# Kernel optimization log

Measured on AMD Instinct MI355X. Metric: run time of the kernel, lower is better.

Reference implementation:

```python
import jax, jax.numpy as jnp
import numpy as np
import math

B, C, L, K, DIL = 8, 32, 32768, 11, 10
PAD_SAME = math.ceil(DIL * (K - 1) / 2)   # 'same' padding for deformable conv
PAD_OFF = (K - 1) // 2                    # padding for the offset-predicting conv
EPS = 1e-3


def batchnorm(x, gamma, beta, mean, var):
    # eval-mode BN over channel dim of [B, C, L]
    scale = (gamma / jnp.sqrt(var + EPS))[None, :, None]
    return (x - mean[None, :, None]) * scale + beta[None, :, None]


def conv1d(x, w, b, pad):
    # x: [B, Cin, L], w: [Cout, Cin, K]
    y = jax.lax.conv_general_dilated(x, w, (1,), [(pad, pad)],
                                     dimension_numbers=('NCH', 'OIH', 'NCH'))
    return y + b[None, :, None]


def deform_conv1d(x, offset, w, b, dilation, pad):
    # x: [B, C, L]; offset: [B, L, K] (single offset group); w: [Cout, Cin, K]
    Bn, Cn, Ln = x.shape
    Kn = w.shape[-1]
    base = jnp.arange(Ln, dtype=x.dtype)[:, None] + jnp.arange(Kn, dtype=x.dtype)[None, :] * dilation - pad
    pos = base[None, :, :] + offset                       # [B, L, K] fractional sample positions
    lo = jnp.floor(pos)
    frac = pos - lo
    lo_i = lo.astype(jnp.int32)

    def gather(idx):
        valid = ((idx >= 0) & (idx < Ln)).astype(x.dtype)  # zero padding outside
        idxc = jnp.clip(idx, 0, Ln - 1).reshape(Bn, 1, Ln * Kn)
        g = jnp.take_along_axis(x, idxc, axis=2).reshape(Bn, Cn, Ln, Kn)
        return g * valid[:, None, :, :]

    v_lo = gather(lo_i)
    v_hi = gather(lo_i + 1)
    sampled = v_lo * (1.0 - frac)[:, None, :, :] + v_hi * frac[:, None, :, :]  # [B, C, L, K]
    out = jnp.einsum('bclk,ock->bol', sampled, w) + b[None, :, None]
    return out


def setup_inputs() -> dict:
    key = jax.random.key(0)
    ks = jax.random.split(key, 8)
    f32 = jnp.float32
    small = lambda k, shape: jax.random.normal(k, shape, dtype=f32) * 0.05
    return dict(
        x=jax.random.normal(ks[0], (B, C, L), dtype=f32),
        bn1_gamma=jnp.ones((C,), f32), bn1_beta=jnp.zeros((C,), f32),
        bn1_mean=small(ks[1], (C,)),
        bn1_var=jax.random.uniform(ks[2], (C,), dtype=f32, minval=0.5, maxval=1.5),
        bn2_gamma=jnp.ones((C,), f32), bn2_beta=jnp.zeros((C,), f32),
        bn2_mean=small(ks[3], (C,)),
        bn2_var=jax.random.uniform(ks[4], (C,), dtype=f32, minval=0.5, maxval=1.5),
        off1_w=small(ks[5], (K, C, K)), off1_b=jnp.zeros((K,), f32),
        off2_w=small(ks[6], (K, C, K)), off2_b=jnp.zeros((K,), f32),
        dc1_w=small(ks[7], (C, C, K)), dc1_b=jnp.zeros((C,), f32),
        dc2_w=small(jax.random.fold_in(key, 99), (C, C, K)), dc2_b=jnp.zeros((C,), f32),
    )


def reference(x, bn1_gamma, bn1_beta, bn1_mean, bn1_var,
              bn2_gamma, bn2_beta, bn2_mean, bn2_var,
              off1_w, off1_b, off2_w, off2_b,
              dc1_w, dc1_b, dc2_w, dc2_b):
    act1 = jax.nn.relu(batchnorm(x, bn1_gamma, bn1_beta, bn1_mean, bn1_var))
    off1 = conv1d(act1, off1_w, off1_b, PAD_OFF)          # [B, K, L]
    offset1 = jnp.transpose(off1, (0, 2, 1))              # [B, L, K]
    d1 = deform_conv1d(act1, offset1, dc1_w, dc1_b, DIL, PAD_SAME)
    act2 = jax.nn.relu(batchnorm(d1, bn2_gamma, bn2_beta, bn2_mean, bn2_var))
    off2 = conv1d(act2, off2_w, off2_b, PAD_OFF)
    offset2 = jnp.transpose(off2, (0, 2, 1))
    d2 = deform_conv1d(act2, offset2, dc2_w, dc2_b, DIL, PAD_SAME)
    return d2 + x
```

## Files before the change

kernel.cpp:

```cpp
#include <hip/hip_runtime.h>
#include <hip/hip_bf16.h>

#define NB 8
#define NC 32
#define NL 32768
#define NK 11
#define DIL 10
#define PADS 50
#define PADO 5
#define EPSV 1e-3f

#define TL    256
#define GUARD 14
#define HALO  (PADS + GUARD)
#define SPAN  (TL + 2 * HALO)
#define NCP   40

typedef __attribute__((ext_vector_type(8))) short bf16x8;
typedef __attribute__((ext_vector_type(4))) float f32x4;

#define WMF_SZ  (NK * 2 * 64 * 8)
#define WOMF_SZ (NK * 64 * 8)

__device__ __forceinline__ unsigned short f2bf(float f) {
    unsigned u = __float_as_uint(f);
    u = (u + 0x7FFFu + ((u >> 16) & 1u)) >> 16;
    return (unsigned short)u;
}
__device__ __forceinline__ float bflo(unsigned p) { return __uint_as_float(p << 16); }
__device__ __forceinline__ float bfhi(unsigned p) { return __uint_as_float(p & 0xffff0000u); }

__global__ void prep_k(const float* __restrict__ dc1_w, const float* __restrict__ dc2_w,
                       const float* __restrict__ off1_w, const float* __restrict__ off2_w,
                       unsigned short* __restrict__ wmf1, unsigned short* __restrict__ wmf2,
                       unsigned short* __restrict__ womf1, unsigned short* __restrict__ womf2)
{
    int i = blockIdx.x * 256 + threadIdx.x;
    if (i < 2 * WMF_SZ) {
        const float* w = (i < WMF_SZ) ? dc1_w : dc2_w;
        unsigned short* dst = (i < WMF_SZ) ? wmf1 : wmf2;
        int j = (i < WMF_SZ) ? i : i - WMF_SZ;
        int e = j & 7, lane = (j >> 3) & 63, k2 = j >> 9;
        int k = k2 >> 1, h = k2 & 1;
        int co = h * 16 + (lane & 15);
        int c  = 8 * (lane >> 4) + e;
        dst[j] = f2bf(w[(co * NC + c) * NK + k]);
    } else if (i < 2 * WMF_SZ + 2 * WOMF_SZ) {
        int i2 = i - 2 * WMF_SZ;
        const float* w = (i2 < WOMF_SZ) ? off1_w : off2_w;
        unsigned short* dst = (i2 < WOMF_SZ) ? womf1 : womf2;
        int j = (i2 < WOMF_SZ) ? i2 : i2 - WOMF_SZ;
        int e = j & 7, lane = (j >> 3) & 63, kk = j >> 9;
        int ko = lane & 15;
        int c  = 8 * (lane >> 4) + e;
        dst[j] = (ko < NK) ? f2bf(w[(ko * NC + c) * NK + kk]) : (unsigned short)0;
    }
}

template <int MODE>
__global__ __launch_bounds__(256, 4) void fused_k(
    const float* __restrict__ src,
    const float* __restrict__ bn1g, const float* __restrict__ bn1b,
    const float* __restrict__ bn1m, const float* __restrict__ bn1v,
    const unsigned short* __restrict__ womf,
    const float* __restrict__ offb,
    const unsigned short* __restrict__ wmf,
    const float* __restrict__ dcb,
    const float* __restrict__ bn2g, const float* __restrict__ bn2b,
    const float* __restrict__ bn2m, const float* __restrict__ bn2v,
    const float* __restrict__ resid,
    float* __restrict__ out)
{
    __shared__ unsigned short tile[SPAN * NCP];
    __shared__ float off_lds[TL * 12];

    const int t  = threadIdx.x;
    const int b  = blockIdx.x >> 7;
    const int l0 = (blockIdx.x & 127) * TL;
    const int s0 = l0 - HALO;
    const float* sb = src + (long)b * NC * NL;

    for (int r = t; r < SPAN; r += 256) {
        const int g = s0 + r;
        const bool ok = (g >= 0 && g < NL);
        #pragma unroll
        for (int j = 0; j < 4; ++j) {
            unsigned tmp[4];
            #pragma unroll
            for (int e = 0; e < 4; ++e) {
                const int c0 = j * 8 + 2 * e;
                float v0 = 0.f, v1 = 0.f;
                if (ok) {
                    v0 = sb[(long)c0 * NL + g];
                    v1 = sb[(long)(c0 + 1) * NL + g];
                    if (MODE == 0) {
                        float sc0 = bn1g[c0] * rsqrtf(bn1v[c0] + EPSV);
                        float sh0 = bn1b[c0] - bn1m[c0] * sc0;
                        float sc1 = bn1g[c0 + 1] * rsqrtf(bn1v[c0 + 1] + EPSV);
                        float sh1 = bn1b[c0 + 1] - bn1m[c0 + 1] * sc1;
                        v0 = fmaxf(fmaf(v0, sc0, sh0), 0.f);
                        v1 = fmaxf(fmaf(v1, sc1, sh1), 0.f);
                    }
                }
                tmp[e] = (unsigned)f2bf(v0) | ((unsigned)f2bf(v1) << 16);
            }
            uint4 pk; pk.x = tmp[0]; pk.y = tmp[1]; pk.z = tmp[2]; pk.w = tmp[3];
            *reinterpret_cast<uint4*>(&tile[r * NCP + j * 8]) = pk;
        }
    }
    __syncthreads();

    const int lane = t & 63;
    const int w    = t >> 6;
    const int n    = lane & 15;
    const int q    = lane >> 4;

    float biasq[4];
    #pragma unroll
    for (int j = 0; j < 4; ++j) {
        int ko = 4 * q + j;
        biasq[j] = (ko < NK) ? offb[ko] : 0.f;
    }

    #pragma unroll 1
    for (int lt = 0; lt < 4; ++lt) {
        const int lt0 = w * 64 + lt * 16;
        f32x4 oc = {0.f, 0.f, 0.f, 0.f};
        #pragma unroll 2
        for (int kk = 0; kk < NK; ++kk) {
            const int r = lt0 + n + (HALO - PADO) + kk;
            bf16x8 bfrag = *reinterpret_cast<const bf16x8*>(&tile[r * NCP + 8 * q]);
            bf16x8 afrag = *reinterpret_cast<const bf16x8*>(&womf[(kk * 64 + lane) * 8]);
            oc = __builtin_amdgcn_mfma_f32_16x16x32_bf16(afrag, bfrag, oc, 0, 0, 0);
        }
        if (q < 3) {
            f32x4 ov;
            #pragma unroll
            for (int j = 0; j < 4; ++j) ov[j] = oc[j] + biasq[j];
            *reinterpret_cast<f32x4*>(&off_lds[(lt0 + n) * 12 + 4 * q]) = ov;
        }
    }

    float dA[4], dB[4], sA[4], hA[4], sB[4], hB[4];
    #pragma unroll
    for (int j = 0; j < 4; ++j) {
        const int c0 = 4 * q + j, c1 = c0 + 16;
        dA[j] = dcb[c0]; dB[j] = dcb[c1];
        if (MODE == 0) {
            sA[j] = bn2g[c0] * rsqrtf(bn2v[c0] + EPSV);
            hA[j] = bn2b[c0] - bn2m[c0] * sA[j];
            sB[j] = bn2g[c1] * rsqrtf(bn2v[c1] + EPSV);
            hB[j] = bn2b[c1] - bn2m[c1] * sB[j];
        }
    }

    #pragma unroll 1
    for (int lt = 0; lt < 4; ++lt) {
        const int lt0 = w * 64 + lt * 16;
        const int l   = l0 + lt0 + n;
        f32x4 acc0 = {0.f, 0.f, 0.f, 0.f};
        f32x4 acc1 = {0.f, 0.f, 0.f, 0.f};
        #pragma unroll 1
        for (int k = 0; k < NK; ++k) {
            const float o    = off_lds[(lt0 + n) * 12 + k];
            const float posf = (float)(l + k * DIL - PADS) + o;
            const float rel  = posf - (float)s0;
            const float lf   = floorf(rel);
            const float fr   = rel - lf;
            const int   lr   = (int)lf;
            float sv[8];
            if (lr >= 0 && lr <= SPAN - 2) {
                const uint4 p0 = *reinterpret_cast<const uint4*>(&tile[lr * NCP + 8 * q]);
                const uint4 p1 = *reinterpret_cast<const uint4*>(&tile[(lr + 1) * NCP + 8 * q]);
                const unsigned pa[4] = {p0.x, p0.y, p0.z, p0.w};
                const unsigned pb[4] = {p1.x, p1.y, p1.z, p1.w};
                #pragma unroll
                for (int e = 0; e < 4; ++e) {
                    const float lo0 = bflo(pa[e]), lo1 = bflo(pb[e]);
                    const float hi0 = bfhi(pa[e]), hi1 = bfhi(pb[e]);
                    sv[2 * e]     = fmaf(lo1 - lo0, fr, lo0);
                    sv[2 * e + 1] = fmaf(hi1 - hi0, fr, hi0);
                }
            } else {
                const float lof = floorf(posf);
                const float fr2 = posf - lof;
                const int lo = (int)lof, hi = lo + 1;
                const float ma = (lo >= 0 && lo < NL) ? 1.f : 0.f;
                const float mb = (hi >= 0 && hi < NL) ? 1.f : 0.f;
                const int ia = min(max(lo, 0), NL - 1);
                const int ib = min(max(hi, 0), NL - 1);
                #pragma unroll
                for (int e = 0; e < 8; ++e) {
                    const int c = 8 * q + e;
                    const float* row = sb + (long)c * NL;
                    float a0 = row[ia], a1 = row[ib];
                    if (MODE == 0) {
                        float sc = bn1g[c] * rsqrtf(bn1v[c] + EPSV);
                        float sh = bn1b[c] - bn1m[c] * sc;
                        a0 = fmaxf(fmaf(a0, sc, sh), 0.f);
                        a1 = fmaxf(fmaf(a1, sc, sh), 0.f);
                    }
                    a0 *= ma; a1 *= mb;
                    sv[e] = fmaf(a1 - a0, fr2, a0);
                }
            }
            union { __hip_bfloat162 h2[4]; bf16x8 v; } pk;
            #pragma unroll
            for (int e = 0; e < 4; ++e)
                pk.h2[e] = __float22bfloat162_rn(make_float2(sv[2 * e], sv[2 * e + 1]));
            const bf16x8 a0f = *reinterpret_cast<const bf16x8*>(&wmf[((k * 2 + 0) * 64 + lane) * 8]);
            const bf16x8 a1f = *reinterpret_cast<const bf16x8*>(&wmf[((k * 2 + 1) * 64 + lane) * 8]);
            acc0 = __builtin_amdgcn_mfma_f32_16x16x32_bf16(a0f, pk.v, acc0, 0, 0, 0);
            acc1 = __builtin_amdgcn_mfma_f32_16x16x32_bf16(a1f, pk.v, acc1, 0, 0, 0);
        }
        const long ob = (long)b * NC * NL + l;
        if (MODE == 0) {
            #pragma unroll
            for (int j = 0; j < 4; ++j) {
                const int c0 = 4 * q + j, c1 = c0 + 16;
                out[ob + (long)c0 * NL] = fmaxf(fmaf(acc0[j] + dA[j], sA[j], hA[j]), 0.f);
                out[ob + (long)c1 * NL] = fmaxf(fmaf(acc1[j] + dB[j], sB[j], hB[j]), 0.f);
            }
        } else {
            #pragma unroll
            for (int j = 0; j < 4; ++j) {
                const int c0 = 4 * q + j, c1 = c0 + 16;
                out[ob + (long)c0 * NL] = acc0[j] + dA[j] + resid[ob + (long)c0 * NL];
                out[ob + (long)c1 * NL] = acc1[j] + dB[j] + resid[ob + (long)c1 * NL];
            }
        }
    }
}

extern "C" void kernel_launch(void* const* d_in, const int* in_sizes, int n_in,
                              void* d_out, int out_size, void* d_ws, size_t ws_size,
                              hipStream_t stream)
{
    const float* x      = (const float*)d_in[0];
    const float* bn1_g  = (const float*)d_in[1];
    const float* bn1_b  = (const float*)d_in[2];
    const float* bn1_m  = (const float*)d_in[3];
    const float* bn1_v  = (const float*)d_in[4];
    const float* bn2_g  = (const float*)d_in[5];
    const float* bn2_b  = (const float*)d_in[6];
    const float* bn2_m  = (const float*)d_in[7];
    const float* bn2_v  = (const float*)d_in[8];
    const float* off1_w = (const float*)d_in[9];
    const float* off1_b = (const float*)d_in[10];
    const float* off2_w = (const float*)d_in[11];
    const float* off2_b = (const float*)d_in[12];
    const float* dc1_w  = (const float*)d_in[13];
    const float* dc1_b  = (const float*)d_in[14];
    const float* dc2_w  = (const float*)d_in[15];
    const float* dc2_b  = (const float*)d_in[16];
    float* out = (float*)d_out;

    char* ws = (char*)d_ws;
    float* act2 = (float*)ws;
    unsigned short* wmf1  = (unsigned short*)(ws + (size_t)NB * NC * NL * 4);
    unsigned short* wmf2  = wmf1 + WMF_SZ;
    unsigned short* womf1 = wmf2 + WMF_SZ;
    unsigned short* womf2 = womf1 + WOMF_SZ;

    prep_k<<<(2 * WMF_SZ + 2 * WOMF_SZ + 255) / 256, 256, 0, stream>>>(
        dc1_w, dc2_w, off1_w, off2_w, wmf1, wmf2, womf1, womf2);

    const int grid = NB * (NL / TL);
    fused_k<0><<<grid, 256, 0, stream>>>(x, bn1_g, bn1_b, bn1_m, bn1_v,
                                         womf1, off1_b, wmf1, dc1_b,
                                         bn2_g, bn2_b, bn2_m, bn2_v,
                                         nullptr, act2);
    fused_k<1><<<grid, 256, 0, stream>>>(act2, nullptr, nullptr, nullptr, nullptr,
                                         womf2, off2_b, wmf2, dc2_b,
                                         nullptr, nullptr, nullptr, nullptr,
                                         x, out);
}
```

Before: 206.7 us.

## Halve tile length, swizzle block order, and hoist offset math for fully unrolled sampling

Shrinks the L tile from 256 to 128, so SPAN becomes 256 and each thread loads exactly one row, and raises launch bounds to 5 waves per SIMD. Blocks are swizzled so consecutive block IDs cover different batches. Offset and position math for all taps is computed up front, and a wave-uniform fast path runs a fully unrolled LDS interpolation plus MFMA loop when all taps fall inside the tile. The aim is more concurrent blocks and better instruction overlap, at the cost of a larger relative halo (more redundant loads per output) and higher register pressure.

```diff
diff --git a/kernel.cpp b/kernel.cpp
--- a/kernel.cpp
+++ b/kernel.cpp
@@ -10,7 +10,7 @@
 #define PADO 5
 #define EPSV 1e-3f
 
-#define TL    256
+#define TL    128
 #define GUARD 14
 #define HALO  (PADS + GUARD)
 #define SPAN  (TL + 2 * HALO)
@@ -58,7 +58,7 @@
 }
 
 template <int MODE>
-__global__ __launch_bounds__(256, 4) void fused_k(
+__global__ __launch_bounds__(256, 5) void fused_k(
     const float* __restrict__ src,
     const float* __restrict__ bn1g, const float* __restrict__ bn1b,
     const float* __restrict__ bn1m, const float* __restrict__ bn1v,
@@ -75,13 +75,14 @@
     __shared__ float off_lds[TL * 12];
 
     const int t  = threadIdx.x;
-    const int b  = blockIdx.x >> 7;
-    const int l0 = (blockIdx.x & 127) * TL;
+    const int sw = ((blockIdx.x & 7) << 8) | (blockIdx.x >> 3);
+    const int b  = sw >> 8;
+    const int l0 = (sw & 255) * TL;
     const int s0 = l0 - HALO;
     const float* sb = src + (long)b * NC * NL;
 
-    for (int r = t; r < SPAN; r += 256) {
-        const int g = s0 + r;
+    {
+        const int g = s0 + t;
         const bool ok = (g >= 0 && g < NL);
         #pragma unroll
         for (int j = 0; j < 4; ++j) {
@@ -102,10 +103,11 @@
                         v1 = fmaxf(fmaf(v1, sc1, sh1), 0.f);
                     }
                 }
-                tmp[e] = (unsigned)f2bf(v0) | ((unsigned)f2bf(v1) << 16);
+                __hip_bfloat162 p2 = __float22bfloat162_rn(make_float2(v0, v1));
+                tmp[e] = *reinterpret_cast<unsigned*>(&p2);
             }
             uint4 pk; pk.x = tmp[0]; pk.y = tmp[1]; pk.z = tmp[2]; pk.w = tmp[3];
-            *reinterpret_cast<uint4*>(&tile[r * NCP + j * 8]) = pk;
+            *reinterpret_cast<uint4*>(&tile[t * NCP + j * 8]) = pk;
         }
     }
     __syncthreads();
@@ -123,10 +125,10 @@
     }
 
     #pragma unroll 1
-    for (int lt = 0; lt < 4; ++lt) {
-        const int lt0 = w * 64 + lt * 16;
+    for (int lt = 0; lt < 2; ++lt) {
+        const int lt0 = w * 32 + lt * 16;
         f32x4 oc = {0.f, 0.f, 0.f, 0.f};
-        #pragma unroll 2
+        #pragma unroll
         for (int kk = 0; kk < NK; ++kk) {
             const int r = lt0 + n + (HALO - PADO) + kk;
             bf16x8 bfrag = *reinterpret_cast<const bf16x8*>(&tile[r * NCP + 8 * q]);
@@ -155,40 +157,67 @@
     }
 
     #pragma unroll 1
-    for (int lt = 0; lt < 4; ++lt) {
-        const int lt0 = w * 64 + lt * 16;
+    for (int lt = 0; lt < 2; ++lt) {
+        const int lt0 = w * 32 + lt * 16;
         const int l   = l0 + lt0 + n;
         f32x4 acc0 = {0.f, 0.f, 0.f, 0.f};
         f32x4 acc1 = {0.f, 0.f, 0.f, 0.f};
-        #pragma unroll 1
+
+        const f32x4 ov0 = *reinterpret_cast<const f32x4*>(&off_lds[(lt0 + n) * 12 + 0]);
+        const f32x4 ov1 = *reinterpret_cast<const f32x4*>(&off_lds[(lt0 + n) * 12 + 4]);
+        const f32x4 ov2 = *reinterpret_cast<const f32x4*>(&off_lds[(lt0 + n) * 12 + 8]);
+
+        float oar[NK], frr[NK];
+        int   lrr[NK];
+        bool  okl = true;
+        #pragma unroll
         for (int k = 0; k < NK; ++k) {
-            const float o    = off_lds[(lt0 + n) * 12 + k];
+            const float o = (k < 4) ? ov0[k & 3] : (k < 8) ? ov1[k & 3] : ov2[k & 3];
+            oar[k] = o;
             const float posf = (float)(l + k * DIL - PADS) + o;
             const float rel  = posf - (float)s0;
             const float lf   = floorf(rel);
-            const float fr   = rel - lf;
-            const int   lr   = (int)lf;
-            float sv[8];
-            if (lr >= 0 && lr <= SPAN - 2) {
+            frr[k] = rel - lf;
+            lrr[k] = (int)lf;
+            okl = okl && (lrr[k] >= 0) && (lrr[k] <= SPAN - 2);
+        }
+
+        if (__all(okl)) {
+            #pragma unroll
+            for (int k = 0; k < NK; ++k) {
+                const int   lr = lrr[k];
+                const float fr = frr[k];
                 const uint4 p0 = *reinterpret_cast<const uint4*>(&tile[lr * NCP + 8 * q]);
                 const uint4 p1 = *reinterpret_cast<const uint4*>(&tile[(lr + 1) * NCP + 8 * q]);
                 const unsigned pa[4] = {p0.x, p0.y, p0.z, p0.w};
                 const unsigned pb[4] = {p1.x, p1.y, p1.z, p1.w};
+                union { __hip_bfloat162 h2[4]; bf16x8 v; } pk;
                 #pragma unroll
                 for (int e = 0; e < 4; ++e) {
                     const float lo0 = bflo(pa[e]), lo1 = bflo(pb[e]);
                     const float hi0 = bfhi(pa[e]), hi1 = bfhi(pb[e]);
-                    sv[2 * e]     = fmaf(lo1 - lo0, fr, lo0);
-                    sv[2 * e + 1] = fmaf(hi1 - hi0, fr, hi0);
+                    const float sA_ = fmaf(lo1 - lo0, fr, lo0);
+                    const float sB_ = fmaf(hi1 - hi0, fr, hi0);
+                    pk.h2[e] = __float22bfloat162_rn(make_float2(sA_, sB_));
                 }
-            } else {
-                const float lof = floorf(posf);
-                const float fr2 = posf - lof;
+                const bf16x8 a0f = *reinterpret_cast<const bf16x8*>(&wmf[((k * 2 + 0) * 64 + lane) * 8]);
+                const bf16x8 a1f = *reinterpret_cast<const bf16x8*>(&wmf[((k * 2 + 1) * 64 + lane) * 8]);
+                acc0 = __builtin_amdgcn_mfma_f32_16x16x32_bf16(a0f, pk.v, acc0, 0, 0, 0);
+                acc1 = __builtin_amdgcn_mfma_f32_16x16x32_bf16(a1f, pk.v, acc1, 0, 0, 0);
+            }
+        } else {
+            #pragma unroll 1
+            for (int k = 0; k < NK; ++k) {
+                const float o    = off_lds[(lt0 + n) * 12 + k];
+                const float posf = (float)(l + k * DIL - PADS) + o;
+                const float lof  = floorf(posf);
+                const float fr2  = posf - lof;
                 const int lo = (int)lof, hi = lo + 1;
                 const float ma = (lo >= 0 && lo < NL) ? 1.f : 0.f;
                 const float mb = (hi >= 0 && hi < NL) ? 1.f : 0.f;
                 const int ia = min(max(lo, 0), NL - 1);
                 const int ib = min(max(hi, 0), NL - 1);
+                float sv[8];
                 #pragma unroll
                 for (int e = 0; e < 8; ++e) {
                     const int c = 8 * q + e;
@@ -203,16 +232,17 @@
                     a0 *= ma; a1 *= mb;
                     sv[e] = fmaf(a1 - a0, fr2, a0);
                 }
-            }
-            union { __hip_bfloat162 h2[4]; bf16x8 v; } pk;
-            #pragma unroll
-            for (int e = 0; e < 4; ++e)
-                pk.h2[e] = __float22bfloat162_rn(make_float2(sv[2 * e], sv[2 * e + 1]));
-            const bf16x8 a0f = *reinterpret_cast<const bf16x8*>(&wmf[((k * 2 + 0) * 64 + lane) * 8]);
-            const bf16x8 a1f = *reinterpret_cast<const bf16x8*>(&wmf[((k * 2 + 1) * 64 + lane) * 8]);
-            acc0 = __builtin_amdgcn_mfma_f32_16x16x32_bf16(a0f, pk.v, acc0, 0, 0, 0);
-            acc1 = __builtin_amdgcn_mfma_f32_16x16x32_bf16(a1f, pk.v, acc1, 0, 0, 0);
-        }
+                union { __hip_bfloat162 h2[4]; bf16x8 v; } pk;
+                #pragma unroll
+                for (int e = 0; e < 4; ++e)
+                    pk.h2[e] = __float22bfloat162_rn(make_float2(sv[2 * e], sv[2 * e + 1]));
+                const bf16x8 a0f = *reinterpret_cast<const bf16x8*>(&wmf[((k * 2 + 0) * 64 + lane) * 8]);
+                const bf16x8 a1f = *reinterpret_cast<const bf16x8*>(&wmf[((k * 2 + 1) * 64 + lane) * 8]);
+                acc0 = __builtin_amdgcn_mfma_f32_16x16x32_bf16(a0f, pk.v, acc0, 0, 0, 0);
+                acc1 = __builtin_amdgcn_mfma_f32_16x16x32_bf16(a1f, pk.v, acc1, 0, 0, 0);
+            }
+        }
+
         const long ob = (long)b * NC * NL + l;
         if (MODE == 0) {
             #pragma unroll
```

Measured after the change: 287.6 us. 39.1% more time.
